# Kernel optimization log

Measured on AMD Instinct MI355X. Metric: run time of the kernel, lower is better.

## Reference

```python
import jax, jax.numpy as jnp
import numpy as np

HEADS = 8


def _attn_1d(xs, w_qkv, w_proj, heads, scale):
    """xs: [N, C, L] -> [N, C, L]. 1x1 conv == channel matmul."""
    n, c, l = xs.shape
    inner = w_proj.shape[1]
    d = inner // heads
    qkv = jnp.einsum('oc,ncl->nol', w_qkv, xs)          # [N, 3*inner, L]
    q, k, v = jnp.split(qkv, 3, axis=1)                  # each [N, inner, L]
    # [N, heads, L, d]
    q = q.reshape(n, heads, d, l).transpose(0, 1, 3, 2)
    k = k.reshape(n, heads, d, l).transpose(0, 1, 3, 2)
    v = v.reshape(n, heads, d, l).transpose(0, 1, 3, 2)
    attn = jax.nn.softmax(jnp.einsum('nhid,nhjd->nhij', q, k) * scale, axis=-1)
    out = jnp.einsum('nhij,nhjd->nhid', attn, v)         # [N, heads, L, d]
    out = out.transpose(0, 1, 3, 2).reshape(n, inner, l) # [N, inner, L]
    return jnp.einsum('co,nol->ncl', w_proj, out)


def _axial(x, w_qkv, w_proj, heads, scale, axis):
    b, c, h, w = x.shape
    if axis == 'h':
        xs = x.transpose(0, 3, 1, 2).reshape(b * w, c, h)
        out = _attn_1d(xs, w_qkv, w_proj, heads, scale)
        return out.reshape(b, w, c, h).transpose(0, 2, 3, 1)
    else:
        xs = x.transpose(0, 2, 1, 3).reshape(b * h, c, w)
        out = _attn_1d(xs, w_qkv, w_proj, heads, scale)
        return out.reshape(b, h, c, w).transpose(0, 2, 1, 3)


def setup_inputs() -> dict:
    key = jax.random.key(0)
    k1, k2, k3 = jax.random.split(key, 3)
    B, C, H, W = 4, 512, 128, 128
    heads = HEADS
    head_dim = C // heads
    inner = head_dim * heads
    x = jax.random.normal(k1, (B, C, H, W), dtype=jnp.float32)
    w_qkv = jax.random.normal(k2, (inner * 3, C), dtype=jnp.float32) * 0.02
    w_proj = jax.random.normal(k3, (C, inner), dtype=jnp.float32) * 0.02
    return {"x": x, "w_qkv": w_qkv, "w_proj": w_proj}


def reference(x, w_qkv, w_proj):
    c = x.shape[1]
    head_dim = c // HEADS
    scale = head_dim ** (-0.5)
    h_out = _axial(x, w_qkv, w_proj, HEADS, scale, 'h')
    w_out = _axial(h_out, w_qkv, w_proj, HEADS, scale, 'w')
    return x + w_out
```

## Files before the change

kernel.cpp:

```cpp
#include <hip/hip_runtime.h>
#include <hip/hip_bf16.h>
#include <stdint.h>

#define B_ 4
#define S_ 128
#define CH 512

typedef __attribute__((ext_vector_type(8))) __bf16 bf16x8;
typedef __attribute__((ext_vector_type(4))) float  f32x4;

__device__ __forceinline__ unsigned short f2b(float f) {
    union { float f; unsigned u; } v; v.f = f;
    unsigned r = v.u + 0x7FFFu + ((v.u >> 16) & 1u);
    return (unsigned short)(r >> 16);
}

#define GLD_LDS16(gp, lp) \
    __builtin_amdgcn_global_load_lds((const __attribute__((address_space(1))) void*)(gp), \
                                     (__attribute__((address_space(3))) void*)(lp), 16, 0, 0)

__global__ void cvt_w(const float* __restrict__ wq, const float* __restrict__ wp,
                      unsigned short* __restrict__ wqb, unsigned short* __restrict__ wpb) {
    int idx = (blockIdx.x * 256 + threadIdx.x) * 4;
    const float* s; unsigned short* d; int off;
    if (idx < 1536 * 512) { s = wq; d = wqb; off = idx; }
    else                  { s = wp; d = wpb; off = idx - 1536 * 512; }
    float4 v = *(const float4*)(s + off);
    ushort4 o; o.x = f2b(v.x); o.y = f2b(v.y); o.z = f2b(v.z); o.w = f2b(v.w);
    *(ushort4*)(d + off) = o;
}

__global__ __launch_bounds__(256) void k0_tr(const float* __restrict__ x,
                                             unsigned short* __restrict__ xb) {
    __shared__ unsigned short t[64][72];
    int bid = blockIdx.x;
    int ct = bid & 7, wt = (bid >> 3) & 1, h = (bid >> 4) & 127, b = bid >> 11;
    int tid = threadIdx.x;
    int c0 = ct * 64, w0 = wt * 64;
    const float* xp = x + ((size_t)b * CH * S_ + h) * S_;
    int wl = (tid & 15) * 4;
#pragma unroll
    for (int it = 0; it < 4; ++it) {
        int c = it * 16 + (tid >> 4);
        float4 v = *(const float4*)(xp + (size_t)(c0 + c) * (S_ * S_) + w0 + wl);
        t[wl + 0][c] = f2b(v.x);
        t[wl + 1][c] = f2b(v.y);
        t[wl + 2][c] = f2b(v.z);
        t[wl + 3][c] = f2b(v.w);
    }
    __syncthreads();
#pragma unroll
    for (int it = 0; it < 2; ++it) {
        int w = it * 32 + (tid >> 3);
        int ce = (tid & 7) * 8;
        int4 v = *(const int4*)&t[w][ce];
        size_t p = (size_t)((b * 128 + w0 + w) * 128 + h);
        *(int4*)(xb + p * 512 + c0 + ce) = v;
    }
}

template<int EPI>
__global__ __launch_bounds__(256) void gemm_tn(
    const unsigned short* __restrict__ A,
    const unsigned short* __restrict__ Bm,
    unsigned short* __restrict__ outb,
    const float* __restrict__ xres,
    float* __restrict__ outf,
    int Mtiles)
{
    __shared__ unsigned short As[128 * 32];
    __shared__ unsigned short Bs[128 * 32];
    int bid = blockIdx.x;
    int mb = bid % Mtiles, nb = bid / Mtiles;
    int m0 = mb * 128, n0 = nb * 128;
    int tid = threadIdx.x, lane = tid & 63, wv = tid >> 6;
    int mw = (wv >> 1) * 64, nw = (wv & 1) * 64;
    f32x4 acc[4][4] = {};

    int jr = lane >> 2;
    int jc = (lane & 3) * 8;
    for (int kt = 0; kt < 16; ++kt) {
        int k0 = kt * 32;
        __syncthreads();
        for (int j = wv * 2; j < wv * 2 + 2; ++j) {
            GLD_LDS16(A  + (size_t)(m0 + j * 16 + jr) * 512 + k0 + jc, As + j * 512);
            GLD_LDS16(Bm + (size_t)(n0 + j * 16 + jr) * 512 + k0 + jc, Bs + j * 512);
        }
        __syncthreads();
        int ko = (lane >> 4) * 8;
        bf16x8 af[4], bfr[4];
#pragma unroll
        for (int mt = 0; mt < 4; ++mt)
            af[mt] = *(const bf16x8*)(As + (mw + mt * 16 + (lane & 15)) * 32 + ko);
#pragma unroll
        for (int nt = 0; nt < 4; ++nt)
            bfr[nt] = *(const bf16x8*)(Bs + (nw + nt * 16 + (lane & 15)) * 32 + ko);
#pragma unroll
        for (int mt = 0; mt < 4; ++mt)
#pragma unroll
            for (int nt = 0; nt < 4; ++nt)
                acc[mt][nt] = __builtin_amdgcn_mfma_f32_16x16x32_bf16(af[mt], bfr[nt], acc[mt][nt], 0, 0, 0);
    }

#pragma unroll
    for (int mt = 0; mt < 4; ++mt) {
        int row0 = m0 + mw + mt * 16 + ((lane >> 4) << 2);
#pragma unroll
        for (int nt = 0; nt < 4; ++nt) {
            int col = n0 + nw + nt * 16 + (lane & 15);
            int i = col & 127, sq = (col >> 7) & 127, bb = col >> 14;
            if (EPI == 0) {
                int g = row0 >> 6, d0 = row0 & 63;
                if (g < 16) {
                    size_t base = ((size_t)(g * 4 + bb) * 16384 + (size_t)sq * 128 + i) * 64 + d0;
                    ushort4 o;
                    o.x = f2b(acc[mt][nt][0]); o.y = f2b(acc[mt][nt][1]);
                    o.z = f2b(acc[mt][nt][2]); o.w = f2b(acc[mt][nt][3]);
                    *(ushort4*)(outb + base) = o;
                } else {
                    size_t base = ((size_t)(g * 4 + bb) * 8192 + (size_t)sq * 64 + d0) * 128 + i;
                    outb[base]       = f2b(acc[mt][nt][0]);
                    outb[base + 128] = f2b(acc[mt][nt][1]);
                    outb[base + 256] = f2b(acc[mt][nt][2]);
                    outb[base + 384] = f2b(acc[mt][nt][3]);
                }
            } else if (EPI == 1) {
                size_t p2 = ((size_t)bb * 128 + i) * 128 + sq;
                ushort4 o;
                o.x = f2b(acc[mt][nt][0]); o.y = f2b(acc[mt][nt][1]);
                o.z = f2b(acc[mt][nt][2]); o.w = f2b(acc[mt][nt][3]);
                *(ushort4*)(outb + p2 * 512 + row0) = o;
            } else {
                size_t base = (((size_t)bb * 512 + row0) * 128 + sq) * 128 + i;
#pragma unroll
                for (int r = 0; r < 4; ++r) {
                    size_t a_ = base + (size_t)r * 16384;
                    outf[a_] = xres[a_] + acc[mt][nt][r];
                }
            }
        }
    }
}

__global__ __launch_bounds__(256) void attn_k(const unsigned short* __restrict__ qkv,
                                              unsigned short* __restrict__ o2) {
    __shared__ unsigned short Qs[128 * 80];
    __shared__ unsigned short Ks[128 * 80];
    __shared__ unsigned short Vt[64 * 144];
    int bid = blockIdx.x;
    int t = bid & 7, sq = (bid >> 3) & 127, b = bid >> 10;
    int tid = threadIdx.x, lane = tid & 63, wv = tid >> 6;
    const unsigned short* qg = qkv + ((size_t)(t * 4 + b) * 16384 + (size_t)sq * 128) * 64;
    const unsigned short* kg = qkv + ((size_t)((8 + t) * 4 + b) * 16384 + (size_t)sq * 128) * 64;
    const unsigned short* vg = qkv + ((size_t)((16 + t) * 4 + b) * 8192 + (size_t)sq * 64) * 128;
    {
        int r = tid >> 3, d0 = (tid & 7) * 8;
#pragma unroll
        for (int it = 0; it < 4; ++it) {
            *(int4*)(Qs + (it * 32 + r) * 80 + d0) = *(const int4*)(qg + (it * 32 + r) * 64 + d0);
            *(int4*)(Ks + (it * 32 + r) * 80 + d0) = *(const int4*)(kg + (it * 32 + r) * 64 + d0);
        }
        int r2 = tid >> 4, i0 = (tid & 15) * 8;
#pragma unroll
        for (int it = 0; it < 4; ++it)
            *(int4*)(Vt + (it * 16 + r2) * 144 + i0) = *(const int4*)(vg + (it * 16 + r2) * 128 + i0);
    }
    __syncthreads();

    f32x4 st[8][2] = {};
#pragma unroll
    for (int kk = 0; kk < 2; ++kk) {
        int ko = kk * 32 + (lane >> 4) * 8;
        bf16x8 bq[2];
#pragma unroll
        for (int nt = 0; nt < 2; ++nt)
            bq[nt] = *(const bf16x8*)(Qs + (wv * 32 + nt * 16 + (lane & 15)) * 80 + ko);
#pragma unroll
        for (int mt = 0; mt < 8; ++mt) {
            bf16x8 ak = *(const bf16x8*)(Ks + (mt * 16 + (lane & 15)) * 80 + ko);
#pragma unroll
            for (int nt = 0; nt < 2; ++nt)
                st[mt][nt] = __builtin_amdgcn_mfma_f32_16x16x32_bf16(ak, bq[nt], st[mt][nt], 0, 0, 0);
        }
    }

    const float sc = 0.125f * 1.44269504088896f;
    float mx[2], rinv[2];
    unsigned ppk[8][2][2];
#pragma unroll
    for (int nt = 0; nt < 2; ++nt) {
        float m = -3.0e38f;
#pragma unroll
        for (int mt = 0; mt < 8; ++mt)
#pragma unroll
            for (int r = 0; r < 4; ++r)
                m = fmaxf(m, st[mt][nt][r]);
        m = fmaxf(m, __shfl_xor(m, 16));
        m = fmaxf(m, __shfl_xor(m, 32));
        mx[nt] = m * sc;
    }
#pragma unroll
    for (int nt = 0; nt < 2; ++nt) {
        float s = 0.f;
#pragma unroll
        for (int mt = 0; mt < 8; ++mt) {
            float p0 = exp2f(st[mt][nt][0] * sc - mx[nt]);
            float p1 = exp2f(st[mt][nt][1] * sc - mx[nt]);
            float p2 = exp2f(st[mt][nt][2] * sc - mx[nt]);
            float p3 = exp2f(st[mt][nt][3] * sc - mx[nt]);
            s += (p0 + p1) + (p2 + p3);
            ppk[mt][nt][0] = (unsigned)f2b(p0) | ((unsigned)f2b(p1) << 16);
            ppk[mt][nt][1] = (unsigned)f2b(p2) | ((unsigned)f2b(p3) << 16);
        }
        s += __shfl_xor(s, 16);
        s += __shfl_xor(s, 32);
        rinv[nt] = 1.0f / s;
    }

    f32x4 ov[4][2] = {};
    int g = lane >> 4;
    int ls0 = (lane & 15) | ((g & 1) << 5);
    int ls1 = ls0 | 16;
    int hi = g >> 1;
#pragma unroll
    for (int kt = 0; kt < 4; ++kt) {
        bf16x8 bp[2];
#pragma unroll
        for (int nt = 0; nt < 2; ++nt) {
            unsigned a0 = (unsigned)__shfl((int)ppk[2 * kt    ][nt][0], ls0);
            unsigned b0 = (unsigned)__shfl((int)ppk[2 * kt + 1][nt][0], ls0);
            unsigned a1 = (unsigned)__shfl((int)ppk[2 * kt    ][nt][1], ls0);
            unsigned b1 = (unsigned)__shfl((int)ppk[2 * kt + 1][nt][1], ls0);
            unsigned a2 = (unsigned)__shfl((int)ppk[2 * kt    ][nt][0], ls1);
            unsigned b2 = (unsigned)__shfl((int)ppk[2 * kt + 1][nt][0], ls1);
            unsigned a3 = (unsigned)__shfl((int)ppk[2 * kt    ][nt][1], ls1);
            unsigned b3 = (unsigned)__shfl((int)ppk[2 * kt + 1][nt][1], ls1);
            union { unsigned u[4]; bf16x8 v; } pk;
            pk.u[0] = hi ? b0 : a0;
            pk.u[1] = hi ? b1 : a1;
            pk.u[2] = hi ? b2 : a2;
            pk.u[3] = hi ? b3 : a3;
            bp[nt] = pk.v;
        }
#pragma unroll
        for (int dt = 0; dt < 4; ++dt) {
            bf16x8 av = *(const bf16x8*)(Vt + (dt * 16 + (lane & 15)) * 144 + kt * 32 + (lane >> 4) * 8);
#pragma unroll
            for (int nt = 0; nt < 2; ++nt)
                ov[dt][nt] = __builtin_amdgcn_mfma_f32_16x16x32_bf16(av, bp[nt], ov[dt][nt], 0, 0, 0);
        }
    }

#pragma unroll
    for (int dt = 0; dt < 4; ++dt) {
        int d0 = dt * 16 + (lane >> 4) * 4;
#pragma unroll
        for (int nt = 0; nt < 2; ++nt) {
            int i = wv * 32 + nt * 16 + (lane & 15);
            size_t p = ((size_t)(b * 128 + sq)) * 128 + i;
            ushort4 o;
            o.x = f2b(ov[dt][nt][0] * rinv[nt]);
            o.y = f2b(ov[dt][nt][1] * rinv[nt]);
            o.z = f2b(ov[dt][nt][2] * rinv[nt]);
            o.w = f2b(ov[dt][nt][3] * rinv[nt]);
            *(ushort4*)(o2 + p * 512 + t * 64 + d0) = o;
        }
    }
}

extern "C" void kernel_launch(void* const* d_in, const int* in_sizes, int n_in,
                              void* d_out, int out_size, void* d_ws, size_t ws_size,
                              hipStream_t stream) {
    const float* x  = (const float*)d_in[0];
    const float* wq = (const float*)d_in[1];
    const float* wp = (const float*)d_in[2];
    float* out = (float*)d_out;
    char* ws = (char*)d_ws;
    unsigned short* wqb = (unsigned short*)(ws);
    unsigned short* wpb = (unsigned short*)(ws + ((size_t)2 << 20));
    unsigned short* xb  = (unsigned short*)(ws + ((size_t)4 << 20));
    unsigned short* o2  = (unsigned short*)(ws + ((size_t)68 << 20));
    unsigned short* qkv = (unsigned short*)(ws + ((size_t)132 << 20));

    cvt_w<<<1024, 256, 0, stream>>>(wq, wp, wqb, wpb);
    k0_tr<<<8192, 256, 0, stream>>>(x, xb);
    gemm_tn<0><<<12 * 512, 256, 0, stream>>>(wqb, xb, qkv, nullptr, nullptr, 12);
    attn_k<<<4096, 256, 0, stream>>>(qkv, o2);
    gemm_tn<1><<<4 * 512, 256, 0, stream>>>(wpb, o2, xb, nullptr, nullptr, 4);
    gemm_tn<0><<<12 * 512, 256, 0, stream>>>(wqb, xb, qkv, nullptr, nullptr, 12);
    attn_k<<<4096, 256, 0, stream>>>(qkv, o2);
    gemm_tn<2><<<4 * 512, 256, 0, stream>>>(wpb, o2, nullptr, x, out, 4);
}
```

Before: 654.9 us.

## Double-buffer GEMM LDS tiles and remap workgroups across XCDs

Adds a second LDS buffer for the A and B tiles so the async global-to-LDS load of the next K slice is issued before the MFMAs on the current slice, replacing two barriers per iteration with one. It also swizzles the block index so consecutive tiles land on the same XCD for better L2 reuse, and precomputes base pointers. The cost is doubled LDS use per block, which may lower occupancy. The remap assumes the grid size is divisible by 8.

```diff
diff --git a/kernel.cpp b/kernel.cpp
--- a/kernel.cpp
+++ b/kernel.cpp
@@ -68,10 +68,11 @@
     float* __restrict__ outf,
     int Mtiles)
 {
-    __shared__ unsigned short As[128 * 32];
-    __shared__ unsigned short Bs[128 * 32];
-    int bid = blockIdx.x;
-    int mb = bid % Mtiles, nb = bid / Mtiles;
+    __shared__ unsigned short As[2][128 * 32];
+    __shared__ unsigned short Bs[2][128 * 32];
+    int nwg = gridDim.x;
+    int wg = (blockIdx.x & 7) * (nwg >> 3) + (blockIdx.x >> 3);
+    int mb = wg % Mtiles, nb = wg / Mtiles;
     int m0 = mb * 128, n0 = nb * 128;
     int tid = threadIdx.x, lane = tid & 63, wv = tid >> 6;
     int mw = (wv >> 1) * 64, nw = (wv & 1) * 64;
@@ -79,28 +80,41 @@
 
     int jr = lane >> 2;
     int jc = (lane & 3) * 8;
+    int j0 = wv * 2;
+
+    const unsigned short* Ab = A  + (size_t)(m0 + j0 * 16 + jr) * 512 + jc;
+    const unsigned short* Bb = Bm + (size_t)(n0 + j0 * 16 + jr) * 512 + jc;
+
+#define STAGE(buf, kt) do {                                                   \
+        int _k0 = (kt) * 32;                                                  \
+        GLD_LDS16(Ab + _k0,        &As[buf][ j0      * 512]);                 \
+        GLD_LDS16(Ab + _k0 + 8192, &As[buf][(j0 + 1) * 512]);                 \
+        GLD_LDS16(Bb + _k0,        &Bs[buf][ j0      * 512]);                 \
+        GLD_LDS16(Bb + _k0 + 8192, &Bs[buf][(j0 + 1) * 512]);                 \
+    } while (0)
+
+    STAGE(0, 0);
+    __syncthreads();
+    int cur = 0;
     for (int kt = 0; kt < 16; ++kt) {
-        int k0 = kt * 32;
-        __syncthreads();
-        for (int j = wv * 2; j < wv * 2 + 2; ++j) {
-            GLD_LDS16(A  + (size_t)(m0 + j * 16 + jr) * 512 + k0 + jc, As + j * 512);
-            GLD_LDS16(Bm + (size_t)(n0 + j * 16 + jr) * 512 + k0 + jc, Bs + j * 512);
-        }
-        __syncthreads();
+        if (kt < 15) STAGE(cur ^ 1, kt + 1);
         int ko = (lane >> 4) * 8;
         bf16x8 af[4], bfr[4];
 #pragma unroll
         for (int mt = 0; mt < 4; ++mt)
-            af[mt] = *(const bf16x8*)(As + (mw + mt * 16 + (lane & 15)) * 32 + ko);
+            af[mt] = *(const bf16x8*)(&As[cur][(mw + mt * 16 + (lane & 15)) * 32 + ko]);
 #pragma unroll
         for (int nt = 0; nt < 4; ++nt)
-            bfr[nt] = *(const bf16x8*)(Bs + (nw + nt * 16 + (lane & 15)) * 32 + ko);
+            bfr[nt] = *(const bf16x8*)(&Bs[cur][(nw + nt * 16 + (lane & 15)) * 32 + ko]);
 #pragma unroll
         for (int mt = 0; mt < 4; ++mt)
 #pragma unroll
             for (int nt = 0; nt < 4; ++nt)
                 acc[mt][nt] = __builtin_amdgcn_mfma_f32_16x16x32_bf16(af[mt], bfr[nt], acc[mt][nt], 0, 0, 0);
-    }
+        __syncthreads();
+        cur ^= 1;
+    }
+#undef STAGE
 
 #pragma unroll
     for (int mt = 0; mt < 4; ++mt) {
```

Result: slower. 713.5 us (+8.9%).

## Rewrite GEMM as 256x256 tile, 8-wave kernel with double-buffered async LDS loads

Applied to the files above, without the earlier changes.

Replaces the 128x128, 4-wave GEMM with a 256x256 tile, 512-thread kernel. It double-buffers K=64 slices in LDS using global_load_lds prefetch interleaved across four sub-quadrants, with fine-grained vmcnt waits and setprio around the MFMA bursts. It also adds an XOR swizzle against LDS bank conflicts and a workgroup remapping for L2 locality. The aim is to hide global load latency, which the old single-buffered loop with two barriers per K step exposed, and to raise data reuse per tile. In exchange it uses 128KB of LDS and many more accumulator registers, which limits occupancy.

```diff
diff --git a/kernel.cpp b/kernel.cpp
--- a/kernel.cpp
+++ b/kernel.cpp
@@ -60,7 +60,7 @@
 }
 
 template<int EPI>
-__global__ __launch_bounds__(256) void gemm_tn(
+__global__ __launch_bounds__(512, 2) void gemm8(
     const unsigned short* __restrict__ A,
     const unsigned short* __restrict__ Bm,
     unsigned short* __restrict__ outb,
@@ -68,74 +68,125 @@
     float* __restrict__ outf,
     int Mtiles)
 {
-    __shared__ unsigned short As[128 * 32];
-    __shared__ unsigned short Bs[128 * 32];
-    int bid = blockIdx.x;
-    int mb = bid % Mtiles, nb = bid / Mtiles;
-    int m0 = mb * 128, n0 = nb * 128;
-    int tid = threadIdx.x, lane = tid & 63, wv = tid >> 6;
-    int mw = (wv >> 1) * 64, nw = (wv & 1) * 64;
-    f32x4 acc[4][4] = {};
-
-    int jr = lane >> 2;
-    int jc = (lane & 3) * 8;
-    for (int kt = 0; kt < 16; ++kt) {
-        int k0 = kt * 32;
-        __syncthreads();
-        for (int j = wv * 2; j < wv * 2 + 2; ++j) {
-            GLD_LDS16(A  + (size_t)(m0 + j * 16 + jr) * 512 + k0 + jc, As + j * 512);
-            GLD_LDS16(Bm + (size_t)(n0 + j * 16 + jr) * 512 + k0 + jc, Bs + j * 512);
-        }
-        __syncthreads();
-        int ko = (lane >> 4) * 8;
-        bf16x8 af[4], bfr[4];
-#pragma unroll
-        for (int mt = 0; mt < 4; ++mt)
-            af[mt] = *(const bf16x8*)(As + (mw + mt * 16 + (lane & 15)) * 32 + ko);
-#pragma unroll
-        for (int nt = 0; nt < 4; ++nt)
-            bfr[nt] = *(const bf16x8*)(Bs + (nw + nt * 16 + (lane & 15)) * 32 + ko);
-#pragma unroll
-        for (int mt = 0; mt < 4; ++mt)
-#pragma unroll
-            for (int nt = 0; nt < 4; ++nt)
-                acc[mt][nt] = __builtin_amdgcn_mfma_f32_16x16x32_bf16(af[mt], bfr[nt], acc[mt][nt], 0, 0, 0);
-    }
-
-#pragma unroll
-    for (int mt = 0; mt < 4; ++mt) {
-        int row0 = m0 + mw + mt * 16 + ((lane >> 4) << 2);
-#pragma unroll
-        for (int nt = 0; nt < 4; ++nt) {
-            int col = n0 + nw + nt * 16 + (lane & 15);
+    __shared__ unsigned short lds[65536];
+    const int NT = 8;
+    int nwg = gridDim.x;
+    int wg = (blockIdx.x & 7) * (nwg >> 3) + (blockIdx.x >> 3);
+    int mb = wg % Mtiles, nb = wg / Mtiles;
+    int m0 = mb * 256, n0 = nb * 256;
+    int tid = threadIdx.x, lane = tid & 63, wid = tid >> 6;
+    int wm = wid >> 2, wn = wid & 3;
+
+    f32x4 acc[8][4] = {};
+
+    int l15  = lane & 15;
+    int rsw  = ((lane >> 2) & 1) << 4;
+    int cA0  = ((lane >> 4) * 8) ^ rsw;
+    int cA1  = (32 + (lane >> 4) * 8) ^ rsw;
+    int arow = (wm * 64 + l15) * 64;
+    int brow = (wn * 32 + l15) * 64;
+
+    int srow = tid >> 3;
+    int scol = ((tid & 7) * 8) ^ (((srow >> 2) & 1) << 4);
+    const unsigned short* Ab0 = A  + (size_t)(m0 + srow) * 512 + scol;
+    const unsigned short* Bb0 = Bm + (size_t)(n0 + (srow >> 5) * 64 + (srow & 31)) * 512 + scol;
+
+#define STAGE_A(kt, reg) do {                                                  \
+        unsigned short* lb_ = &lds[((((kt) & 1) * 2 + (reg)) * 8192)];         \
+        const unsigned short* g_ = Ab0 + (size_t)(reg) * (64 * 512) + (kt) * 64;\
+        GLD_LDS16(g_,             lb_ + wid * 512);                            \
+        GLD_LDS16(g_ + 128 * 512, lb_ + 4096 + wid * 512);                     \
+    } while (0)
+#define STAGE_B(kt, reg) do {                                                  \
+        unsigned short* lb_ = &lds[32768 + ((((kt) & 1) * 2 + (reg)) * 8192)]; \
+        const unsigned short* g_ = Bb0 + (size_t)(reg) * (32 * 512) + (kt) * 64;\
+        GLD_LDS16(g_,             lb_ + wid * 512);                            \
+        GLD_LDS16(g_ + 128 * 512, lb_ + 4096 + wid * 512);                     \
+    } while (0)
+
+    STAGE_A(0, 0); STAGE_A(0, 1); STAGE_B(0, 0); STAGE_B(0, 1);
+    STAGE_A(1, 0); STAGE_B(1, 0);
+    asm volatile("s_waitcnt vmcnt(4)" ::: "memory");
+    __builtin_amdgcn_s_barrier();
+
+    for (int j = 0; j < NT; ++j) {
+        int db = j & 1;
+#pragma unroll
+        for (int q = 0; q < 4; ++q) {
+            const int mq = q >> 1, nq = q & 1;
+            int abase = (db * 2 + mq) * 8192 + arow;
+            int bbase = 32768 + (db * 2 + nq) * 8192 + brow;
+            bf16x8 af[4][2], bq[2][2];
+#pragma unroll
+            for (int fr = 0; fr < 4; ++fr) {
+                af[fr][0] = *(const bf16x8*)&lds[abase + fr * 1024 + cA0];
+                af[fr][1] = *(const bf16x8*)&lds[abase + fr * 1024 + cA1];
+            }
+#pragma unroll
+            for (int fb = 0; fb < 2; ++fb) {
+                bq[fb][0] = *(const bf16x8*)&lds[bbase + fb * 1024 + cA0];
+                bq[fb][1] = *(const bf16x8*)&lds[bbase + fb * 1024 + cA1];
+            }
+            if (q == 0)      { if (j + 1 < NT) STAGE_A(j + 1, 1); }
+            else if (q == 1) { if (j + 1 < NT) STAGE_B(j + 1, 1); }
+            else if (q == 2) { if (j + 2 < NT) STAGE_A(j + 2, 0); }
+            else {
+                if (j + 2 < NT) STAGE_B(j + 2, 0);
+                if (j < NT - 2) asm volatile("s_waitcnt vmcnt(4)" ::: "memory");
+                else            asm volatile("s_waitcnt vmcnt(0)" ::: "memory");
+            }
+            __builtin_amdgcn_s_barrier();
+            asm volatile("s_waitcnt lgkmcnt(0)" ::: "memory");
+            __builtin_amdgcn_s_setprio(1);
+#pragma unroll
+            for (int fr = 0; fr < 4; ++fr)
+#pragma unroll
+                for (int fb = 0; fb < 2; ++fb) {
+                    acc[mq * 4 + fr][nq * 2 + fb] = __builtin_amdgcn_mfma_f32_16x16x32_bf16(
+                        af[fr][0], bq[fb][0], acc[mq * 4 + fr][nq * 2 + fb], 0, 0, 0);
+                    acc[mq * 4 + fr][nq * 2 + fb] = __builtin_amdgcn_mfma_f32_16x16x32_bf16(
+                        af[fr][1], bq[fb][1], acc[mq * 4 + fr][nq * 2 + fb], 0, 0, 0);
+                }
+            __builtin_amdgcn_s_setprio(0);
+            __builtin_amdgcn_s_barrier();
+        }
+    }
+#undef STAGE_A
+#undef STAGE_B
+
+#pragma unroll
+    for (int mi = 0; mi < 8; ++mi) {
+        int row0 = m0 + wm * 128 + (mi >> 2) * 64 + (mi & 3) * 16 + ((lane >> 4) << 2);
+#pragma unroll
+        for (int ni = 0; ni < 4; ++ni) {
+            int col = n0 + wn * 64 + (ni >> 1) * 32 + (ni & 1) * 16 + (lane & 15);
             int i = col & 127, sq = (col >> 7) & 127, bb = col >> 14;
+            f32x4 a4 = acc[mi][ni];
             if (EPI == 0) {
                 int g = row0 >> 6, d0 = row0 & 63;
                 if (g < 16) {
                     size_t base = ((size_t)(g * 4 + bb) * 16384 + (size_t)sq * 128 + i) * 64 + d0;
                     ushort4 o;
-                    o.x = f2b(acc[mt][nt][0]); o.y = f2b(acc[mt][nt][1]);
-                    o.z = f2b(acc[mt][nt][2]); o.w = f2b(acc[mt][nt][3]);
+                    o.x = f2b(a4[0]); o.y = f2b(a4[1]); o.z = f2b(a4[2]); o.w = f2b(a4[3]);
                     *(ushort4*)(outb + base) = o;
                 } else {
                     size_t base = ((size_t)(g * 4 + bb) * 8192 + (size_t)sq * 64 + d0) * 128 + i;
-                    outb[base]       = f2b(acc[mt][nt][0]);
-                    outb[base + 128] = f2b(acc[mt][nt][1]);
-                    outb[base + 256] = f2b(acc[mt][nt][2]);
-                    outb[base + 384] = f2b(acc[mt][nt][3]);
+                    outb[base]       = f2b(a4[0]);
+                    outb[base + 128] = f2b(a4[1]);
+                    outb[base + 256] = f2b(a4[2]);
+                    outb[base + 384] = f2b(a4[3]);
                 }
             } else if (EPI == 1) {
                 size_t p2 = ((size_t)bb * 128 + i) * 128 + sq;
                 ushort4 o;
-                o.x = f2b(acc[mt][nt][0]); o.y = f2b(acc[mt][nt][1]);
-                o.z = f2b(acc[mt][nt][2]); o.w = f2b(acc[mt][nt][3]);
+                o.x = f2b(a4[0]); o.y = f2b(a4[1]); o.z = f2b(a4[2]); o.w = f2b(a4[3]);
                 *(ushort4*)(outb + p2 * 512 + row0) = o;
             } else {
                 size_t base = (((size_t)bb * 512 + row0) * 128 + sq) * 128 + i;
 #pragma unroll
                 for (int r = 0; r < 4; ++r) {
                     size_t a_ = base + (size_t)r * 16384;
-                    outf[a_] = xres[a_] + acc[mt][nt][r];
+                    outf[a_] = xres[a_] + a4[r];
                 }
             }
         }
@@ -284,10 +335,10 @@
 
     cvt_w<<<1024, 256, 0, stream>>>(wq, wp, wqb, wpb);
     k0_tr<<<8192, 256, 0, stream>>>(x, xb);
-    gemm_tn<0><<<12 * 512, 256, 0, stream>>>(wqb, xb, qkv, nullptr, nullptr, 12);
+    gemm8<0><<<6 * 256, 512, 0, stream>>>(wqb, xb, qkv, nullptr, nullptr, 6);
     attn_k<<<4096, 256, 0, stream>>>(qkv, o2);
-    gemm_tn<1><<<4 * 512, 256, 0, stream>>>(wpb, o2, xb, nullptr, nullptr, 4);
-    gemm_tn<0><<<12 * 512, 256, 0, stream>>>(wqb, xb, qkv, nullptr, nullptr, 12);
+    gemm8<1><<<2 * 256, 512, 0, stream>>>(wpb, o2, xb, nullptr, nullptr, 2);
+    gemm8<0><<<6 * 256, 512, 0, stream>>>(wqb, xb, qkv, nullptr, nullptr, 6);
     attn_k<<<4096, 256, 0, stream>>>(qkv, o2);
-    gemm_tn<2><<<4 * 512, 256, 0, stream>>>(wpb, o2, nullptr, x, out, 4);
-}
+    gemm8<2><<<2 * 256, 512, 0, stream>>>(wpb, o2, nullptr, x, out, 2);
+}
```

After: 635.0 us. 3.0% less time.
